# Performance work log

Measured on AMD Instinct MI355X. Metric: run time of the kernel, lower is better.

## Reference

```python
import jax, jax.numpy as jnp
import numpy as np

B, S, J, D = 64, 2048, 25, 3
FEAT_DIM = 128
COMPUTED = 12  # pos(3) + vel(3) + acc(3) + angles(3)
IN_MLP = COMPUTED * J  # 300
HID = FEAT_DIM * 2     # 256
CONN = np.array([(0, 1), (1, 5), (1, 6), (5, 7), (7, 9), (6, 8), (8, 10),
                 (1, 11), (1, 12), (11, 13), (13, 15), (12, 14), (14, 16)], dtype=np.int32)


def setup_inputs() -> dict:
    key = jax.random.key(0)
    ks = jax.random.split(key, 8)
    return {
        "poses": jax.random.normal(ks[0], (B, S, J, D), dtype=jnp.float32),
        "W1": jax.random.normal(ks[1], (IN_MLP, HID), dtype=jnp.float32) * 0.05,
        "b1": jnp.zeros((HID,), jnp.float32),
        "gamma": jnp.ones((HID,), jnp.float32),
        "beta": jnp.zeros((HID,), jnp.float32),
        "running_mean": jnp.zeros((HID,), jnp.float32),
        "running_var": jnp.ones((HID,), jnp.float32),
        "W2": jax.random.normal(ks[2], (HID, FEAT_DIM), dtype=jnp.float32) * 0.05,
        "b2": jnp.zeros((FEAT_DIM,), jnp.float32),
        "joint_weights": jnp.ones((J,), jnp.float32),
    }


def reference(poses, W1, b1, gamma, beta, running_mean, running_var, W2, b2, joint_weights):
    b, s, j, d = poses.shape
    # --- root-centering + max-distance normalization ---
    p = poses - poses[:, :, 0:1, :]
    dist = jnp.linalg.norm(p, axis=-1, keepdims=True)           # [B,S,J,1]
    max_dist = jnp.max(dist, axis=2, keepdims=True)             # [B,S,1,1]
    p = p / (max_dist + 1e-8)
    # --- velocity / acceleration (zero-padded first frames) ---
    zpad = jnp.zeros_like(p[:, :1])
    vel = jnp.concatenate([zpad, p[:, 1:] - p[:, :-1]], axis=1)
    acc = jnp.concatenate([zpad, vel[:, 1:] - vel[:, :-1]], axis=1)
    # --- joint angles: vectorized gather + normalize + acos (replaces B*S*13 python loop) ---
    v1 = p[:, :, CONN[:, 1], :] - p[:, :, CONN[:, 0], :]        # [B,S,13,3]
    vnorm = jnp.maximum(jnp.linalg.norm(v1, axis=-1, keepdims=True), 1e-12)  # F.normalize eps
    ang = jnp.arccos(jnp.clip(v1 / vnorm, -1.0, 1.0))           # [B,S,13,3]
    ang = ang.reshape(b, s, -1)                                 # [B,S,39]
    pad = jnp.zeros((b, s, j * 3 - ang.shape[-1]), ang.dtype)   # pad to J*3=75
    angles = jnp.concatenate([ang, pad], axis=-1).reshape(b, s, j, 3)
    # --- combine, weight, project ---
    feat = jnp.concatenate([p, vel, acc, angles], axis=-1)      # [B,S,J,12]
    feat = feat * joint_weights.reshape(1, 1, j, 1)
    x = feat.reshape(b * s, -1)                                 # [B*S,300]
    x = x @ W1 + b1
    x = gamma * (x - running_mean) / jnp.sqrt(running_var + 1e-5) + beta  # BN eval mode
    x = jax.nn.relu(x)                                          # dropout = identity (eval)
    x = x @ W2 + b2
    return x.reshape(b, s, -1)                                  # [B,S,128]
```

## Files before the change

kernel.cpp:

```cpp
#include <hip/hip_runtime.h>
#include <hip/hip_bf16.h>
#include <stdint.h>


#define S_    2048
#define MT_   64
#define HID_  256
#define OUT_  128

typedef __attribute__((ext_vector_type(8))) short   short8;
typedef __attribute__((ext_vector_type(4))) float   floatx4;

__constant__ int d_c0[13] = {0,1,1,5,7,6,8,1,1,11,13,12,14};
__constant__ int d_c1[13] = {1,5,6,7,9,8,10,11,12,13,15,14,16};

__device__ __forceinline__ unsigned short bf16_bits(float v) {
    union { float f; unsigned u; } x; x.f = v;
    unsigned r = x.u + 0x7fffu + ((x.u >> 16) & 1u);
    return (unsigned short)(r >> 16);
}

__device__ __forceinline__ float facos(float x) {
    float ax = fabsf(x);
    float p = fmaf(ax, -0.0187293f, 0.0742610f);
    p = fmaf(ax, p, -0.2121144f);
    p = fmaf(ax, p, 1.5707288f);
    float r = sqrtf(1.f - ax) * p;
    return x < 0.f ? 3.14159265358979f - r : r;
}

__global__ void prep_kernel(const float* __restrict__ W1, const float* __restrict__ b1,
                            const float* __restrict__ gamma, const float* __restrict__ beta,
                            const float* __restrict__ rmean, const float* __restrict__ rvar,
                            const float* __restrict__ W2,
                            unsigned short* __restrict__ w1p,
                            unsigned short* __restrict__ w2p,
                            float* __restrict__ b1p) {
    int idx = blockIdx.x * 256 + threadIdx.x;
    int lane = idx & 63;
    if (idx < 10240) {
        int blk = idx >> 6;
        int kc = blk >> 4, nt = blk & 15;
        int n  = nt * 16 + (lane & 15);
        int k0 = kc * 32 + (lane >> 4) * 8;
        float a = gamma[n] * rsqrtf(rvar[n] + 1e-5f);
        short8 v;
        #pragma unroll
        for (int j = 0; j < 8; j++) {
            int k = k0 + j;
            float w = (k < 300) ? W1[k * HID_ + n] * a : 0.f;
            v[j] = (short)bf16_bits(w);
        }
        *(short8*)(w1p + blk * 512 + lane * 8) = v;
    } else if (idx < 14336) {
        int blk = (idx - 10240) >> 6;
        int kc = blk >> 3, nt = blk & 7;
        int n  = nt * 16 + (lane & 15);
        int k0 = kc * 32 + (lane >> 4) * 8;
        short8 v;
        #pragma unroll
        for (int j = 0; j < 8; j++)
            v[j] = (short)bf16_bits(W2[(k0 + j) * OUT_ + n]);
        *(short8*)(w2p + blk * 512 + lane * 8) = v;
    } else if (idx < 14592) {
        int n = idx - 14336;
        float a = gamma[n] * rsqrtf(rvar[n] + 1e-5f);
        b1p[n] = fmaf(a, b1[n] - rmean[n], beta[n]);
    }
}

#define LDS_FEAT 0
#define LDS_RS   41984
#define LDS_RSM  (LDS_RS + 66 * 16)
#define LDS_TOT  (LDS_RSM + 66 * 4 + 8)

__global__ __launch_bounds__(256, 3) void pose_mlp(
    const float* __restrict__ poses,
    const unsigned short* __restrict__ w1p,
    const unsigned short* __restrict__ w2p,
    const float* __restrict__ b1p,
    const float* __restrict__ b2,
    const float* __restrict__ jw,
    float* __restrict__ out)
{
    __shared__ __align__(16) unsigned char smem[LDS_TOT];
    const int tid  = threadIdx.x;
    const int lane = tid & 63;
    const int wv   = tid >> 6;
    const int t0   = blockIdx.x * MT_;
    const int s0   = t0 & (S_ - 1);

    short8 bw[4];
    #pragma unroll
    for (int ni = 0; ni < 4; ni++)
        bw[ni] = *(const short8*)(w1p + (unsigned)(wv * 4 + ni) * 512 + lane * 8);

    unsigned short* feat = (unsigned short*)(smem + LDS_FEAT);
    float4*   rs  = (float4*)(smem + LDS_RS);
    unsigned* rsm = (unsigned*)(smem + LDS_RSM);

    if (tid < 66) rsm[tid] = 0u;
    __syncthreads();
    for (int i = tid; i < 66 * 25; i += 256) {
        int f = i / 25, j = i - f * 25;
        int g = t0 - 2 + f; if (g < 0) g = 0;
        const float* P = poses + (size_t)g * 75;
        float dx = P[j*3]   - P[0];
        float dy = P[j*3+1] - P[1];
        float dz = P[j*3+2] - P[2];
        float d2 = fmaf(dx, dx, fmaf(dy, dy, dz * dz));
        atomicMax(&rsm[f], __float_as_uint(d2));
    }
    __syncthreads();
    if (tid < 66) {
        int g = t0 - 2 + tid; if (g < 0) g = 0;
        const float* P = poses + (size_t)g * 75;
        float sc = 1.f / (sqrtf(__uint_as_float(rsm[tid])) + 1e-8f);
        rs[tid] = make_float4(P[0], P[1], P[2], sc);
    }
    __syncthreads();

    for (int i = tid; i < MT_ * 25; i += 256) {
        int tt = i / 25, j = i - tt * 25;
        int s  = s0 + tt;
        int g  = t0 + tt;
        int g1 = g - 1 < 0 ? 0 : g - 1;
        int g2 = g - 2 < 0 ? 0 : g - 2;
        const float* Pc = poses + (size_t)g  * 75 + j * 3;
        const float* P1 = poses + (size_t)g1 * 75 + j * 3;
        const float* P2 = poses + (size_t)g2 * 75 + j * 3;
        float4 rc = rs[tt + 2], rm = rs[tt + 1], rp = rs[tt];
        float cx = (Pc[0] - rc.x) * rc.w, cy = (Pc[1] - rc.y) * rc.w, cz = (Pc[2] - rc.z) * rc.w;
        float mx = (P1[0] - rm.x) * rm.w, my = (P1[1] - rm.y) * rm.w, mz = (P1[2] - rm.z) * rm.w;
        float px = (P2[0] - rp.x) * rp.w, py = (P2[1] - rp.y) * rp.w, pz = (P2[2] - rp.z) * rp.w;
        bool h1 = (s >= 1), h2 = (s >= 2);
        float vx = h1 ? cx - mx : 0.f, vy = h1 ? cy - my : 0.f, vz = h1 ? cz - mz : 0.f;
        float ux = h2 ? mx - px : 0.f, uy = h2 ? my - py : 0.f, uz = h2 ? mz - pz : 0.f;
        float qx = vx - ux, qy = vy - uy, qz = vz - uz;
        float w = jw[j];
        unsigned short o0 = bf16_bits(cx * w), o1 = bf16_bits(cy * w), o2 = bf16_bits(cz * w);
        unsigned short o3 = bf16_bits(vx * w), o4 = bf16_bits(vy * w), o5 = bf16_bits(vz * w);
        unsigned short o6 = bf16_bits(qx * w), o7 = bf16_bits(qy * w), o8 = bf16_bits(qz * w);
        unsigned base = tt * 328 + j * 12;
        *(unsigned*)(feat + base)     = (unsigned)o0 | ((unsigned)o1 << 16);
        *(unsigned*)(feat + base + 2) = (unsigned)o2 | ((unsigned)o3 << 16);
        *(unsigned*)(feat + base + 4) = (unsigned)o4 | ((unsigned)o5 << 16);
        *(unsigned*)(feat + base + 6) = (unsigned)o6 | ((unsigned)o7 << 16);
        feat[base + 8] = o8;
    }

    for (int i = tid; i < MT_ * 13; i += 256) {
        int tt = i / 13, e = i - tt * 13;
        int g  = t0 + tt;
        const float* A = poses + (size_t)g * 75 + d_c1[e] * 3;
        const float* B = poses + (size_t)g * 75 + d_c0[e] * 3;
        float vx = A[0] - B[0], vy = A[1] - B[1], vz = A[2] - B[2];
        float n  = sqrtf(fmaf(vx, vx, fmaf(vy, vy, vz * vz)));
        float inv = 1.f / fmaxf(n, 1e-12f);
        float w = jw[e];
        float a0 = facos(fminf(fmaxf(vx * inv, -1.f), 1.f)) * w;
        float a1 = facos(fminf(fmaxf(vy * inv, -1.f), 1.f)) * w;
        float a2 = facos(fminf(fmaxf(vz * inv, -1.f), 1.f)) * w;
        unsigned base = tt * 328 + e * 12 + 9;
        feat[base] = bf16_bits(a0);
        *(unsigned*)(feat + base + 1) = (unsigned)bf16_bits(a1) | ((unsigned)bf16_bits(a2) << 16);
    }

    for (int i = tid; i < MT_ * 64; i += 256) {
        int tt = i >> 6, z = i & 63;
        int k;
        if (z < 36) { int jj = z / 3; k = (13 + jj) * 12 + 9 + (z - jj * 3); }
        else        { k = 300 + z - 36; }
        feat[tt * 328 + k] = 0;
    }
    __syncthreads();

    floatx4 acc[4][4];
    #pragma unroll
    for (int mi = 0; mi < 4; mi++)
        #pragma unroll
        for (int ni = 0; ni < 4; ni++) acc[mi][ni] = (floatx4){0.f, 0.f, 0.f, 0.f};

    #pragma unroll 1
    for (int kc = 0; kc < 10; kc++) {
        short8 bn[4];
        if (kc < 9) {
            #pragma unroll
            for (int ni = 0; ni < 4; ni++)
                bn[ni] = *(const short8*)(w1p + (unsigned)((kc + 1) * 16 + wv * 4 + ni) * 512 + lane * 8);
        }
        short8 af[4];
        #pragma unroll
        for (int mi = 0; mi < 4; mi++)
            af[mi] = *(const short8*)(feat + (mi * 16 + (lane & 15)) * 328 + kc * 32 + (lane >> 4) * 8);
        #pragma unroll
        for (int mi = 0; mi < 4; mi++)
            #pragma unroll
            for (int ni = 0; ni < 4; ni++)
                acc[mi][ni] = __builtin_amdgcn_mfma_f32_16x16x32_bf16(
                    af[mi], bw[ni], acc[mi][ni], 0, 0, 0);
        if (kc < 9) {
            #pragma unroll
            for (int ni = 0; ni < 4; ni++) bw[ni] = bn[ni];
        }
    }

    short8 bw2[2];
    #pragma unroll
    for (int ni = 0; ni < 2; ni++)
        bw2[ni] = *(const short8*)(w2p + (unsigned)(wv * 2 + ni) * 512 + lane * 8);

    __syncthreads();

    unsigned short* hid = feat;
    float bv[4];
    #pragma unroll
    for (int ni = 0; ni < 4; ni++) bv[ni] = b1p[wv * 64 + ni * 16 + (lane & 15)];
    #pragma unroll
    for (int mi = 0; mi < 4; mi++)
        #pragma unroll
        for (int ni = 0; ni < 4; ni++)
            #pragma unroll
            for (int r = 0; r < 4; r++) {
                float v = fmaxf(acc[mi][ni][r] + bv[ni], 0.f);
                int m   = mi * 16 + (lane >> 4) * 4 + r;
                int col = wv * 64 + ni * 16 + (lane & 15);
                hid[m * 264 + col] = bf16_bits(v);
            }
    __syncthreads();

    floatx4 acc2[4][2];
    #pragma unroll
    for (int mi = 0; mi < 4; mi++)
        #pragma unroll
        for (int ni = 0; ni < 2; ni++) acc2[mi][ni] = (floatx4){0.f, 0.f, 0.f, 0.f};

    #pragma unroll 1
    for (int kc = 0; kc < 8; kc++) {
        short8 bn2[2];
        if (kc < 7) {
            #pragma unroll
            for (int ni = 0; ni < 2; ni++)
                bn2[ni] = *(const short8*)(w2p + (unsigned)((kc + 1) * 8 + wv * 2 + ni) * 512 + lane * 8);
        }
        short8 af[4];
        #pragma unroll
        for (int mi = 0; mi < 4; mi++)
            af[mi] = *(const short8*)(hid + (mi * 16 + (lane & 15)) * 264 + kc * 32 + (lane >> 4) * 8);
        #pragma unroll
        for (int mi = 0; mi < 4; mi++)
            #pragma unroll
            for (int ni = 0; ni < 2; ni++)
                acc2[mi][ni] = __builtin_amdgcn_mfma_f32_16x16x32_bf16(
                    af[mi], bw2[ni], acc2[mi][ni], 0, 0, 0);
        if (kc < 7) {
            #pragma unroll
            for (int ni = 0; ni < 2; ni++) bw2[ni] = bn2[ni];
        }
    }

    float c2[2];
    #pragma unroll
    for (int ni = 0; ni < 2; ni++) c2[ni] = b2[wv * 32 + ni * 16 + (lane & 15)];
    #pragma unroll
    for (int mi = 0; mi < 4; mi++)
        #pragma unroll
        for (int ni = 0; ni < 2; ni++)
            #pragma unroll
            for (int r = 0; r < 4; r++) {
                int m   = mi * 16 + (lane >> 4) * 4 + r;
                int col = wv * 32 + ni * 16 + (lane & 15);
                out[(size_t)(t0 + m) * OUT_ + col] = acc2[mi][ni][r] + c2[ni];
            }
}

extern "C" void kernel_launch(void* const* d_in, const int* in_sizes, int n_in,
                              void* d_out, int out_size, void* d_ws, size_t ws_size,
                              hipStream_t stream) {
    (void)in_sizes; (void)n_in; (void)out_size; (void)ws_size;
    const float* poses = (const float*)d_in[0];
    const float* W1    = (const float*)d_in[1];
    const float* b1    = (const float*)d_in[2];
    const float* gamma = (const float*)d_in[3];
    const float* beta  = (const float*)d_in[4];
    const float* rmean = (const float*)d_in[5];
    const float* rvar  = (const float*)d_in[6];
    const float* W2    = (const float*)d_in[7];
    const float* b2    = (const float*)d_in[8];
    const float* jw    = (const float*)d_in[9];

    unsigned short* w1p = (unsigned short*)d_ws;
    unsigned short* w2p = w1p + 320 * HID_;
    float* b1p = (float*)((char*)d_ws + (320 * HID_ + HID_ * OUT_) * 2);

    prep_kernel<<<57, 256, 0, stream>>>(W1, b1, gamma, beta, rmean, rvar, W2,
                                        w1p, w2p, b1p);
    pose_mlp<<<2048, 256, 0, stream>>>(poses, w1p, w2p, b1p, b2, jw, (float*)d_out);
}
```

Before: 159.7 us.

## Stage root-centered poses in LDS per half-tile and use fast intrinsics

The feature-building phase now loads root-centered poses for 34 frames into shared memory in two 32-frame halves, then computes max distance, position, velocity, acceleration and angles from LDS instead of re-reading global poses several times. Connection indices become packed 64-bit constants, joint weights are cached in LDS, and packed bf16 conversion plus fast sqrt/rcp builtins replace the slower paths. The prep kernel is also rewritten to one element per thread with coalesced reads. Processing in two halves adds extra barriers, and the fast intrinsics may differ slightly in precision.

```diff
diff --git a/kernel.cpp b/kernel.cpp
--- a/kernel.cpp
+++ b/kernel.cpp
@@ -11,13 +11,22 @@
 typedef __attribute__((ext_vector_type(8))) short   short8;
 typedef __attribute__((ext_vector_type(4))) float   floatx4;
 
-__constant__ int d_c0[13] = {0,1,1,5,7,6,8,1,1,11,13,12,14};
-__constant__ int d_c1[13] = {1,5,6,7,9,8,10,11,12,13,15,14,16};
+#define C0M 0x0ECDB118675110ULL
+#define C1M 0x0FDECBA9786540ULL
 
 __device__ __forceinline__ unsigned short bf16_bits(float v) {
     union { float f; unsigned u; } x; x.f = v;
     unsigned r = x.u + 0x7fffu + ((x.u >> 16) & 1u);
     return (unsigned short)(r >> 16);
+}
+
+__device__ __forceinline__ unsigned pkbf16(float a, float b) {
+#if __has_builtin(__builtin_amdgcn_cvt_pk_bf16_f32)
+    auto v = __builtin_amdgcn_cvt_pk_bf16_f32(a, b);
+    unsigned u; __builtin_memcpy(&u, &v, 4); return u;
+#else
+    return (unsigned)bf16_bits(a) | ((unsigned)bf16_bits(b) << 16);
+#endif
 }
 
 __device__ __forceinline__ float facos(float x) {
@@ -25,7 +34,7 @@
     float p = fmaf(ax, -0.0187293f, 0.0742610f);
     p = fmaf(ax, p, -0.2121144f);
     p = fmaf(ax, p, 1.5707288f);
-    float r = sqrtf(1.f - ax) * p;
+    float r = __builtin_amdgcn_sqrtf(1.f - ax) * p;
     return x < 0.f ? 3.14159265358979f - r : r;
 }
 
@@ -37,42 +46,31 @@
                             unsigned short* __restrict__ w2p,
                             float* __restrict__ b1p) {
     int idx = blockIdx.x * 256 + threadIdx.x;
-    int lane = idx & 63;
-    if (idx < 10240) {
-        int blk = idx >> 6;
-        int kc = blk >> 4, nt = blk & 15;
-        int n  = nt * 16 + (lane & 15);
-        int k0 = kc * 32 + (lane >> 4) * 8;
-        float a = gamma[n] * rsqrtf(rvar[n] + 1e-5f);
-        short8 v;
-        #pragma unroll
-        for (int j = 0; j < 8; j++) {
-            int k = k0 + j;
-            float w = (k < 300) ? W1[k * HID_ + n] * a : 0.f;
-            v[j] = (short)bf16_bits(w);
-        }
-        *(short8*)(w1p + blk * 512 + lane * 8) = v;
-    } else if (idx < 14336) {
-        int blk = (idx - 10240) >> 6;
-        int kc = blk >> 3, nt = blk & 7;
-        int n  = nt * 16 + (lane & 15);
-        int k0 = kc * 32 + (lane >> 4) * 8;
-        short8 v;
-        #pragma unroll
-        for (int j = 0; j < 8; j++)
-            v[j] = (short)bf16_bits(W2[(k0 + j) * OUT_ + n]);
-        *(short8*)(w2p + blk * 512 + lane * 8) = v;
-    } else if (idx < 14592) {
-        int n = idx - 14336;
-        float a = gamma[n] * rsqrtf(rvar[n] + 1e-5f);
+    if (idx < 81920) {
+        int k = idx >> 8, n = idx & 255;
+        float a = gamma[n] * __builtin_amdgcn_rsqf(rvar[n] + 1e-5f);
+        float v = (k < 300) ? W1[k * HID_ + n] * a : 0.f;
+        int blk = (k >> 5) * 16 + (n >> 4);
+        int off = blk * 512 + (((k >> 3) & 3) * 16 + (n & 15)) * 8 + (k & 7);
+        w1p[off] = bf16_bits(v);
+    } else if (idx < 114688) {
+        int i2 = idx - 81920;
+        int k = i2 >> 7, n = i2 & 127;
+        int blk = (k >> 5) * 8 + (n >> 4);
+        int off = blk * 512 + (((k >> 3) & 3) * 16 + (n & 15)) * 8 + (k & 7);
+        w2p[off] = bf16_bits(W2[k * OUT_ + n]);
+    } else if (idx < 114944) {
+        int n = idx - 114688;
+        float a = gamma[n] * __builtin_amdgcn_rsqf(rvar[n] + 1e-5f);
         b1p[n] = fmaf(a, b1[n] - rmean[n], beta[n]);
     }
 }
 
 #define LDS_FEAT 0
-#define LDS_RS   41984
-#define LDS_RSM  (LDS_RS + 66 * 16)
-#define LDS_TOT  (LDS_RSM + 66 * 4 + 8)
+#define LDS_PB   41984
+#define LDS_RSM  (LDS_PB + 34 * 76 * 4)
+#define LDS_JW   (LDS_RSM + 34 * 4)
+#define LDS_TOT  (LDS_JW + 25 * 4 + 4)
 
 __global__ __launch_bounds__(256, 3) void pose_mlp(
     const float* __restrict__ poses,
@@ -90,82 +88,18 @@
     const int t0   = blockIdx.x * MT_;
     const int s0   = t0 & (S_ - 1);
 
+    unsigned short* feat = (unsigned short*)(smem + LDS_FEAT);
+    float*    pbuf = (float*)(smem + LDS_PB);
+    unsigned* rsm  = (unsigned*)(smem + LDS_RSM);
+    float*    scl  = (float*)rsm;
+    float*    jwl  = (float*)(smem + LDS_JW);
+
     short8 bw[4];
     #pragma unroll
     for (int ni = 0; ni < 4; ni++)
         bw[ni] = *(const short8*)(w1p + (unsigned)(wv * 4 + ni) * 512 + lane * 8);
 
-    unsigned short* feat = (unsigned short*)(smem + LDS_FEAT);
-    float4*   rs  = (float4*)(smem + LDS_RS);
-    unsigned* rsm = (unsigned*)(smem + LDS_RSM);
-
-    if (tid < 66) rsm[tid] = 0u;
-    __syncthreads();
-    for (int i = tid; i < 66 * 25; i += 256) {
-        int f = i / 25, j = i - f * 25;
-        int g = t0 - 2 + f; if (g < 0) g = 0;
-        const float* P = poses + (size_t)g * 75;
-        float dx = P[j*3]   - P[0];
-        float dy = P[j*3+1] - P[1];
-        float dz = P[j*3+2] - P[2];
-        float d2 = fmaf(dx, dx, fmaf(dy, dy, dz * dz));
-        atomicMax(&rsm[f], __float_as_uint(d2));
-    }
-    __syncthreads();
-    if (tid < 66) {
-        int g = t0 - 2 + tid; if (g < 0) g = 0;
-        const float* P = poses + (size_t)g * 75;
-        float sc = 1.f / (sqrtf(__uint_as_float(rsm[tid])) + 1e-8f);
-        rs[tid] = make_float4(P[0], P[1], P[2], sc);
-    }
-    __syncthreads();
-
-    for (int i = tid; i < MT_ * 25; i += 256) {
-        int tt = i / 25, j = i - tt * 25;
-        int s  = s0 + tt;
-        int g  = t0 + tt;
-        int g1 = g - 1 < 0 ? 0 : g - 1;
-        int g2 = g - 2 < 0 ? 0 : g - 2;
-        const float* Pc = poses + (size_t)g  * 75 + j * 3;
-        const float* P1 = poses + (size_t)g1 * 75 + j * 3;
-        const float* P2 = poses + (size_t)g2 * 75 + j * 3;
-        float4 rc = rs[tt + 2], rm = rs[tt + 1], rp = rs[tt];
-        float cx = (Pc[0] - rc.x) * rc.w, cy = (Pc[1] - rc.y) * rc.w, cz = (Pc[2] - rc.z) * rc.w;
-        float mx = (P1[0] - rm.x) * rm.w, my = (P1[1] - rm.y) * rm.w, mz = (P1[2] - rm.z) * rm.w;
-        float px = (P2[0] - rp.x) * rp.w, py = (P2[1] - rp.y) * rp.w, pz = (P2[2] - rp.z) * rp.w;
-        bool h1 = (s >= 1), h2 = (s >= 2);
-        float vx = h1 ? cx - mx : 0.f, vy = h1 ? cy - my : 0.f, vz = h1 ? cz - mz : 0.f;
-        float ux = h2 ? mx - px : 0.f, uy = h2 ? my - py : 0.f, uz = h2 ? mz - pz : 0.f;
-        float qx = vx - ux, qy = vy - uy, qz = vz - uz;
-        float w = jw[j];
-        unsigned short o0 = bf16_bits(cx * w), o1 = bf16_bits(cy * w), o2 = bf16_bits(cz * w);
-        unsigned short o3 = bf16_bits(vx * w), o4 = bf16_bits(vy * w), o5 = bf16_bits(vz * w);
-        unsigned short o6 = bf16_bits(qx * w), o7 = bf16_bits(qy * w), o8 = bf16_bits(qz * w);
-        unsigned base = tt * 328 + j * 12;
-        *(unsigned*)(feat + base)     = (unsigned)o0 | ((unsigned)o1 << 16);
-        *(unsigned*)(feat + base + 2) = (unsigned)o2 | ((unsigned)o3 << 16);
-        *(unsigned*)(feat + base + 4) = (unsigned)o4 | ((unsigned)o5 << 16);
-        *(unsigned*)(feat + base + 6) = (unsigned)o6 | ((unsigned)o7 << 16);
-        feat[base + 8] = o8;
-    }
-
-    for (int i = tid; i < MT_ * 13; i += 256) {
-        int tt = i / 13, e = i - tt * 13;
-        int g  = t0 + tt;
-        const float* A = poses + (size_t)g * 75 + d_c1[e] * 3;
-        const float* B = poses + (size_t)g * 75 + d_c0[e] * 3;
-        float vx = A[0] - B[0], vy = A[1] - B[1], vz = A[2] - B[2];
-        float n  = sqrtf(fmaf(vx, vx, fmaf(vy, vy, vz * vz)));
-        float inv = 1.f / fmaxf(n, 1e-12f);
-        float w = jw[e];
-        float a0 = facos(fminf(fmaxf(vx * inv, -1.f), 1.f)) * w;
-        float a1 = facos(fminf(fmaxf(vy * inv, -1.f), 1.f)) * w;
-        float a2 = facos(fminf(fmaxf(vz * inv, -1.f), 1.f)) * w;
-        unsigned base = tt * 328 + e * 12 + 9;
-        feat[base] = bf16_bits(a0);
-        *(unsigned*)(feat + base + 1) = (unsigned)bf16_bits(a1) | ((unsigned)bf16_bits(a2) << 16);
-    }
-
+    if (tid < 25) jwl[tid] = jw[tid];
     for (int i = tid; i < MT_ * 64; i += 256) {
         int tt = i >> 6, z = i & 63;
         int k;
@@ -173,7 +107,69 @@
         else        { k = 300 + z - 36; }
         feat[tt * 328 + k] = 0;
     }
-    __syncthreads();
+
+    for (int h = 0; h < 2; h++) {
+        int hb = t0 + 32 * h - 2;
+        if (tid < 34) rsm[tid] = 0u;
+        for (int i = tid; i < 34 * 75; i += 256) {
+            int f = i / 75, r = i - f * 75;
+            int g = hb + f; if (g < 0) g = 0;
+            const float* P = poses + (size_t)g * 75;
+            pbuf[f * 76 + r] = P[r] - P[r - (r / 3) * 3];
+        }
+        __syncthreads();
+        for (int i = tid; i < 34 * 25; i += 256) {
+            int f = i / 25, j = i - f * 25;
+            const float* q = pbuf + f * 76 + j * 3;
+            float d2 = fmaf(q[0], q[0], fmaf(q[1], q[1], q[2] * q[2]));
+            atomicMax(&rsm[f], __float_as_uint(d2));
+        }
+        __syncthreads();
+        if (tid < 34) {
+            float m = __uint_as_float(rsm[tid]);
+            scl[tid] = __builtin_amdgcn_rcpf(__builtin_amdgcn_sqrtf(m) + 1e-8f);
+        }
+        __syncthreads();
+        for (int i = tid; i < 32 * 25; i += 256) {
+            int tt = i / 25, j = i - tt * 25;
+            int s  = s0 + 32 * h + tt;
+            const float* pc = pbuf + (tt + 2) * 76 + j * 3;
+            const float* pm = pc - 76;
+            const float* pp = pc - 152;
+            float sc = scl[tt + 2], sm = scl[tt + 1], sp = scl[tt];
+            float cx = pc[0] * sc, cy = pc[1] * sc, cz = pc[2] * sc;
+            float mx = pm[0] * sm, my = pm[1] * sm, mz = pm[2] * sm;
+            float px = pp[0] * sp, py = pp[1] * sp, pz = pp[2] * sp;
+            bool h1 = (s >= 1), h2 = (s >= 2);
+            float vx = h1 ? cx - mx : 0.f, vy = h1 ? cy - my : 0.f, vz = h1 ? cz - mz : 0.f;
+            float ux = h2 ? mx - px : 0.f, uy = h2 ? my - py : 0.f, uz = h2 ? mz - pz : 0.f;
+            float qx = vx - ux, qy = vy - uy, qz = vz - uz;
+            float w = jwl[j];
+            unsigned base = (unsigned)(32 * h + tt) * 328 + j * 12;
+            *(unsigned*)(feat + base)     = pkbf16(cx * w, cy * w);
+            *(unsigned*)(feat + base + 2) = pkbf16(cz * w, vx * w);
+            *(unsigned*)(feat + base + 4) = pkbf16(vy * w, vz * w);
+            *(unsigned*)(feat + base + 6) = pkbf16(qx * w, qy * w);
+            feat[base + 8] = bf16_bits(qz * w);
+        }
+        for (int i = tid; i < 32 * 13; i += 256) {
+            int tt = i / 13, e = i - tt * 13;
+            const float* pf = pbuf + (tt + 2) * 76;
+            int a0 = (int)((C0M >> (4 * e)) & 15) * 3;
+            int a1 = (((int)((C1M >> (4 * e)) & 15)) + 1) * 3;
+            float vx = pf[a1] - pf[a0], vy = pf[a1+1] - pf[a0+1], vz = pf[a1+2] - pf[a0+2];
+            float d  = fmaf(vx, vx, fmaf(vy, vy, vz * vz));
+            float inv = __builtin_amdgcn_rcpf(fmaxf(__builtin_amdgcn_sqrtf(d), 1e-12f));
+            float w = jwl[e];
+            float A0 = facos(fminf(fmaxf(vx * inv, -1.f), 1.f)) * w;
+            float A1 = facos(fminf(fmaxf(vy * inv, -1.f), 1.f)) * w;
+            float A2 = facos(fminf(fmaxf(vz * inv, -1.f), 1.f)) * w;
+            unsigned base = (unsigned)(32 * h + tt) * 328 + e * 12 + 9;
+            feat[base] = bf16_bits(A0);
+            *(unsigned*)(feat + base + 1) = pkbf16(A1, A2);
+        }
+        __syncthreads();
+    }
 
     floatx4 acc[4][4];
     #pragma unroll
@@ -293,7 +289,7 @@
     unsigned short* w2p = w1p + 320 * HID_;
     float* b1p = (float*)((char*)d_ws + (320 * HID_ + HID_ * OUT_) * 2);
 
-    prep_kernel<<<57, 256, 0, stream>>>(W1, b1, gamma, beta, rmean, rvar, W2,
-                                        w1p, w2p, b1p);
+    prep_kernel<<<449, 256, 0, stream>>>(W1, b1, gamma, beta, rmean, rvar, W2,
+                                         w1p, w2p, b1p);
     pose_mlp<<<2048, 256, 0, stream>>>(poses, w1p, w2p, b1p, b2, jw, (float*)d_out);
 }
```

Result: slower. 174.5 us (+9.3%).
